# Performance work log

Measured on AMD Instinct MI355X. Metric: run time of the kernel, lower is better.

Reference implementation:

```python
import jax, jax.numpy as jnp
import numpy as np

LATENT = 3
POLY = 3
SINDY_DIM = 22  # 3 ones + 3 linear + 6 quad + 10 cubic


def sindy_library(z, poly_order=POLY, latent_dim=LATENT):
    # z: [N, latent_dim] -> [N, sindy_dim]; mirrors the torch loop ordering.
    N = z.shape[0]
    cols = [jnp.ones((N,), z.dtype) for _ in range(latent_dim)]
    if poly_order > 0:
        cols += [z[:, i] for i in range(latent_dim)]
    if poly_order > 1:
        for i in range(latent_dim):
            for j in range(i, latent_dim):
                cols.append(z[:, i] * z[:, j])
    if poly_order > 2:
        for i in range(latent_dim):
            for j in range(i, latent_dim):
                for k in range(j, latent_dim):
                    cols.append(z[:, i] * z[:, j] * z[:, k])
    return jnp.stack(cols, axis=1)


def _xavier(key, out_f, in_f):
    lim = np.sqrt(6.0 / (in_f + out_f)).astype(np.float32)
    return jax.random.uniform(key, (out_f, in_f), jnp.float32, -lim, lim)


def setup_inputs() -> dict:
    key = jax.random.key(0)
    ks = jax.random.split(key, 16)
    N, D = 262144, 128
    we = [128, 64, 32, 3]
    wd = [3, 32, 64, 128]
    d = {}
    d["x"] = jax.random.normal(ks[0], (N, D), jnp.float32)
    d["dx"] = jax.random.normal(ks[1], (N, D), jnp.float32)
    for li, (i_f, o_f) in enumerate(zip(we[:-1], we[1:])):
        d[f"We{li+1}"] = _xavier(ks[2 + li], o_f, i_f)
        d[f"be{li+1}"] = jnp.zeros((o_f,), jnp.float32)
    for li, (i_f, o_f) in enumerate(zip(wd[:-1], wd[1:])):
        d[f"Wd{li+1}"] = _xavier(ks[6 + li], o_f, i_f)
        d[f"bd{li+1}"] = jnp.zeros((o_f,), jnp.float32)
    d["EW"] = jnp.full((LATENT, SINDY_DIM), 0.5, jnp.float32)  # nn.init.constant_(E.weight, 0.5)
    d["Eb"] = jax.random.normal(ks[10], (LATENT,), jnp.float32) * 0.1
    return d


def reference(x, dx, We1, be1, We2, be2, We3, be3,
              Wd1, bd1, Wd2, bd2, Wd3, bd3, EW, Eb):
    # encoder forward (Linear + Identity chain)
    z = ((x @ We1.T + be1) @ We2.T + be2) @ We3.T + be3            # [N, L]
    # encoder Jacobian is constant (pure linear chain): J_enc = We3 @ We2 @ We1
    J_enc = We3 @ We2 @ We1                                        # [L, D]
    dz = dx @ J_enc.T                                              # [N, L]
    # SINDy prediction of z-dot
    theta = sindy_library(z)                                       # [N, SINDY_DIM]
    dzb = theta @ EW.T + Eb                                        # [N, L]
    # decoder forward
    xb = ((z @ Wd1.T + bd1) @ Wd2.T + bd2) @ Wd3.T + bd3           # [N, D]
    # decoder Jacobian (constant)
    J_dec = Wd3 @ Wd2 @ Wd1                                        # [D, L]
    dxb = dzb @ J_dec.T                                            # [N, D]
    return z, dz, dzb, xb, dxb
```

## Files before the change

kernel.cpp:

```cpp
#include <hip/hip_runtime.h>

#define D 128
#define LAT 3
#define SD 22

__global__ __launch_bounds__(256) void fuse_weights(
    const float* __restrict__ We1, const float* __restrict__ be1,
    const float* __restrict__ We2, const float* __restrict__ be2,
    const float* __restrict__ We3, const float* __restrict__ be3,
    const float* __restrict__ Wd1, const float* __restrict__ bd1,
    const float* __restrict__ Wd2, const float* __restrict__ bd2,
    const float* __restrict__ Wd3, const float* __restrict__ bd3,
    float* __restrict__ ws)
{
    __shared__ float A1[3][64];
    __shared__ float B1[64][3];
    __shared__ float t2d[64];
    const int t = threadIdx.x;

    if (t < 192) {
        {
            int r = t >> 6, c = t & 63;
            float s = 0.f;
            #pragma unroll 8
            for (int i = 0; i < 32; ++i) s += We3[r * 32 + i] * We2[i * 64 + c];
            A1[r][c] = s;
        }
        {
            int o = t / 3, l = t - o * 3;
            float s = 0.f;
            #pragma unroll 8
            for (int i = 0; i < 32; ++i) s += Wd2[o * 32 + i] * Wd1[i * 3 + l];
            B1[o][l] = s;
        }
    } else {
        int i = t - 192;
        float s = bd2[i];
        #pragma unroll 8
        for (int j = 0; j < 32; ++j) s += Wd2[i * 32 + j] * bd1[j];
        t2d[i] = s;
    }
    __syncthreads();

    for (int e = t; e < 3 * D; e += 256) {
        int r = e >> 7, c = e & 127;
        float s = 0.f;
        #pragma unroll 8
        for (int j = 0; j < 64; ++j) s += A1[r][j] * We1[j * D + c];
        ws[e] = s;
    }
    if (t < 3) {
        float s = be3[t];
        #pragma unroll 8
        for (int j = 0; j < 64; ++j) s += A1[t][j] * be1[j];
        #pragma unroll 8
        for (int i = 0; i < 32; ++i) s += We3[t * 32 + i] * be2[i];
        ws[384 + t] = s;
    }
    if (t < 128) {
        float s0 = 0.f, s1 = 0.f, s2 = 0.f, sb = bd3[t];
        #pragma unroll 8
        for (int j = 0; j < 64; ++j) {
            float w = Wd3[t * 64 + j];
            s0 += w * B1[j][0];
            s1 += w * B1[j][1];
            s2 += w * B1[j][2];
            sb += w * t2d[j];
        }
        ((float4*)(ws + 512))[t] = make_float4(s0, s1, s2, sb);
    }
}

__global__ __launch_bounds__(256) void sindy_fused(
    const float* __restrict__ x, const float* __restrict__ dx,
    const float* __restrict__ EW, const float* __restrict__ Eb,
    const float* __restrict__ ws, float* __restrict__ out, int nrows)
{
    const int lane = threadIdx.x & 31;
    const int half = threadIdx.x >> 5;

    const float4 je0 = *(const float4*)(ws + 0 * D + lane * 4);
    const float4 je1 = *(const float4*)(ws + 1 * D + lane * 4);
    const float4 je2 = *(const float4*)(ws + 2 * D + lane * 4);
    const float benc0 = ws[384], benc1 = ws[385], benc2 = ws[386];
    const float4 jd0 = ((const float4*)(ws + 512))[lane * 4 + 0];
    const float4 jd1 = ((const float4*)(ws + 512))[lane * 4 + 1];
    const float4 jd2 = ((const float4*)(ws + 512))[lane * 4 + 2];
    const float4 jd3 = ((const float4*)(ws + 512))[lane * 4 + 3];

    float ew[LAT][SD];
    #pragma unroll
    for (int r = 0; r < LAT; ++r)
        #pragma unroll
        for (int k = 0; k < SD; ++k) ew[r][k] = EW[r * SD + k];
    const float eb0 = Eb[0], eb1 = Eb[1], eb2 = Eb[2];

    const int xbBase  = 9 * nrows;
    const int dxbBase = 137 * nrows;
    const int rowsPerGrid = gridDim.x * 8;

    for (int row = blockIdx.x * 8 + half; row < nrows; row += rowsPerGrid) {
        const float4 xv  = *(const float4*)(x  + row * D + lane * 4);
        const float4 dxv = *(const float4*)(dx + row * D + lane * 4);

        float pz0 = je0.x * xv.x + je0.y * xv.y + je0.z * xv.z + je0.w * xv.w;
        float pz1 = je1.x * xv.x + je1.y * xv.y + je1.z * xv.z + je1.w * xv.w;
        float pz2 = je2.x * xv.x + je2.y * xv.y + je2.z * xv.z + je2.w * xv.w;
        float pd0 = je0.x * dxv.x + je0.y * dxv.y + je0.z * dxv.z + je0.w * dxv.w;
        float pd1 = je1.x * dxv.x + je1.y * dxv.y + je1.z * dxv.z + je1.w * dxv.w;
        float pd2 = je2.x * dxv.x + je2.y * dxv.y + je2.z * dxv.z + je2.w * dxv.w;

        #pragma unroll
        for (int m = 16; m >= 1; m >>= 1) {
            pz0 += __shfl_xor(pz0, m);
            pz1 += __shfl_xor(pz1, m);
            pz2 += __shfl_xor(pz2, m);
            pd0 += __shfl_xor(pd0, m);
            pd1 += __shfl_xor(pd1, m);
            pd2 += __shfl_xor(pd2, m);
        }

        const float z0 = pz0 + benc0, z1 = pz1 + benc1, z2 = pz2 + benc2;

        const float q00 = z0 * z0, q01 = z0 * z1, q02 = z0 * z2;
        const float q11 = z1 * z1, q12 = z1 * z2, q22 = z2 * z2;
        float th[SD];
        th[0] = 1.f;  th[1] = 1.f;  th[2] = 1.f;
        th[3] = z0;   th[4] = z1;   th[5] = z2;
        th[6] = q00;  th[7] = q01;  th[8] = q02;
        th[9] = q11;  th[10] = q12; th[11] = q22;
        th[12] = q00 * z0; th[13] = q00 * z1; th[14] = q00 * z2;
        th[15] = q11 * z0; th[16] = q12 * z0; th[17] = q22 * z0;
        th[18] = q11 * z1; th[19] = q11 * z2; th[20] = q22 * z1;
        th[21] = q22 * z2;

        float dzb0 = eb0, dzb1 = eb1, dzb2 = eb2;
        #pragma unroll
        for (int k = 0; k < SD; ++k) {
            dzb0 += ew[0][k] * th[k];
            dzb1 += ew[1][k] * th[k];
            dzb2 += ew[2][k] * th[k];
        }

        const int n3 = row * 3;
        if (lane < 3) {
            const float zv = (lane == 0) ? z0 : (lane == 1) ? z1 : z2;
            const float dv = (lane == 0) ? pd0 : (lane == 1) ? pd1 : pd2;
            const float bv = (lane == 0) ? dzb0 : (lane == 1) ? dzb1 : dzb2;
            out[n3 + lane] = zv;
            out[3 * nrows + n3 + lane] = dv;
            out[6 * nrows + n3 + lane] = bv;
        }

        float4 xbv, dxbv;
        xbv.x = jd0.x * z0 + jd0.y * z1 + jd0.z * z2 + jd0.w;
        xbv.y = jd1.x * z0 + jd1.y * z1 + jd1.z * z2 + jd1.w;
        xbv.z = jd2.x * z0 + jd2.y * z1 + jd2.z * z2 + jd2.w;
        xbv.w = jd3.x * z0 + jd3.y * z1 + jd3.z * z2 + jd3.w;
        dxbv.x = jd0.x * dzb0 + jd0.y * dzb1 + jd0.z * dzb2;
        dxbv.y = jd1.x * dzb0 + jd1.y * dzb1 + jd1.z * dzb2;
        dxbv.z = jd2.x * dzb0 + jd2.y * dzb1 + jd2.z * dzb2;
        dxbv.w = jd3.x * dzb0 + jd3.y * dzb1 + jd3.z * dzb2;

        *(float4*)(out + xbBase  + row * D + lane * 4) = xbv;
        *(float4*)(out + dxbBase + row * D + lane * 4) = dxbv;
    }
}

extern "C" void kernel_launch(void* const* d_in, const int* in_sizes, int n_in,
                              void* d_out, int out_size, void* d_ws, size_t ws_size,
                              hipStream_t stream) {
    const float* x   = (const float*)d_in[0];
    const float* dx  = (const float*)d_in[1];
    const float* We1 = (const float*)d_in[2];
    const float* be1 = (const float*)d_in[3];
    const float* We2 = (const float*)d_in[4];
    const float* be2 = (const float*)d_in[5];
    const float* We3 = (const float*)d_in[6];
    const float* be3 = (const float*)d_in[7];
    const float* Wd1 = (const float*)d_in[8];
    const float* bd1 = (const float*)d_in[9];
    const float* Wd2 = (const float*)d_in[10];
    const float* bd2 = (const float*)d_in[11];
    const float* Wd3 = (const float*)d_in[12];
    const float* bd3 = (const float*)d_in[13];
    const float* EW  = (const float*)d_in[14];
    const float* Eb  = (const float*)d_in[15];

    float* ws  = (float*)d_ws;
    float* out = (float*)d_out;
    const int nrows = in_sizes[0] / D;

    fuse_weights<<<1, 256, 0, stream>>>(We1, be1, We2, be2, We3, be3,
                                        Wd1, bd1, Wd2, bd2, Wd3, bd3, ws);

    sindy_fused<<<2048, 256, 0, stream>>>(x, dx, EW, Eb, ws, out, nrows);
}
```

Measured before the change: 129.0 us.

## Process two rows per half-wave with register-prefetched next iteration loads

Each 32-lane group now handles two rows per iteration (r and r+8) and the block covers 16 rows per step. The x/dx loads for the next iteration are issued before the current rows are computed, a software-pipelined double buffer held in registers. The goal is to hide global load latency in this bandwidth-bound kernel and to interleave two independent shuffle reductions. In exchange it raises register pressure, which can lower occupancy, and the grid stride doubles while the launch size stays the same.

Result: no change. 130.3 us (+1.0%).

```diff
diff --git a/kernel.cpp b/kernel.cpp
--- a/kernel.cpp
+++ b/kernel.cpp
@@ -71,6 +71,45 @@
     }
 }
 
+
+#define EMIT_ROW(ROW, Z0, Z1, Z2, DV0, DV1, DV2)                              \
+  {                                                                           \
+    const float z0 = (Z0) + benc0, z1 = (Z1) + benc1, z2 = (Z2) + benc2;      \
+    const float q00 = z0*z0, q01 = z0*z1, q02 = z0*z2;                        \
+    const float q11 = z1*z1, q12 = z1*z2, q22 = z2*z2;                        \
+    float th[SD];                                                             \
+    th[0]=1.f; th[1]=1.f; th[2]=1.f;                                          \
+    th[3]=z0;  th[4]=z1;  th[5]=z2;                                           \
+    th[6]=q00; th[7]=q01; th[8]=q02; th[9]=q11; th[10]=q12; th[11]=q22;       \
+    th[12]=q00*z0; th[13]=q00*z1; th[14]=q00*z2;                              \
+    th[15]=q11*z0; th[16]=q12*z0; th[17]=q22*z0;                              \
+    th[18]=q11*z1; th[19]=q11*z2; th[20]=q22*z1; th[21]=q22*z2;               \
+    float b0 = eb0, b1 = eb1, b2 = eb2;                                       \
+    _Pragma("unroll")                                                         \
+    for (int k = 0; k < SD; ++k) {                                            \
+      b0 += ew[0][k]*th[k]; b1 += ew[1][k]*th[k]; b2 += ew[2][k]*th[k];       \
+    }                                                                         \
+    if (lane < 3) {                                                           \
+      const float zv = (lane==0) ? z0   : (lane==1) ? z1   : z2;              \
+      const float dv = (lane==0) ? (DV0): (lane==1) ? (DV1): (DV2);           \
+      const float bv = (lane==0) ? b0   : (lane==1) ? b1   : b2;              \
+      out[(ROW)*3 + lane]             = zv;                                   \
+      out[3*nrows + (ROW)*3 + lane]   = dv;                                   \
+      out[6*nrows + (ROW)*3 + lane]   = bv;                                   \
+    }                                                                         \
+    float4 xbv, dxbv;                                                         \
+    xbv.x  = jd0.x*z0 + jd0.y*z1 + jd0.z*z2 + jd0.w;                          \
+    xbv.y  = jd1.x*z0 + jd1.y*z1 + jd1.z*z2 + jd1.w;                          \
+    xbv.z  = jd2.x*z0 + jd2.y*z1 + jd2.z*z2 + jd2.w;                          \
+    xbv.w  = jd3.x*z0 + jd3.y*z1 + jd3.z*z2 + jd3.w;                          \
+    dxbv.x = jd0.x*b0 + jd0.y*b1 + jd0.z*b2;                                  \
+    dxbv.y = jd1.x*b0 + jd1.y*b1 + jd1.z*b2;                                  \
+    dxbv.z = jd2.x*b0 + jd2.y*b1 + jd2.z*b2;                                  \
+    dxbv.w = jd3.x*b0 + jd3.y*b1 + jd3.z*b2;                                  \
+    *(float4*)(out + xbBase  + (ROW)*D + lane*4) = xbv;                       \
+    *(float4*)(out + dxbBase + (ROW)*D + lane*4) = dxbv;                      \
+  }
+
 __global__ __launch_bounds__(256) void sindy_fused(
     const float* __restrict__ x, const float* __restrict__ dx,
     const float* __restrict__ EW, const float* __restrict__ Eb,
@@ -97,73 +136,62 @@
 
     const int xbBase  = 9 * nrows;
     const int dxbBase = 137 * nrows;
-    const int rowsPerGrid = gridDim.x * 8;
-
-    for (int row = blockIdx.x * 8 + half; row < nrows; row += rowsPerGrid) {
-        const float4 xv  = *(const float4*)(x  + row * D + lane * 4);
-        const float4 dxv = *(const float4*)(dx + row * D + lane * 4);
-
-        float pz0 = je0.x * xv.x + je0.y * xv.y + je0.z * xv.z + je0.w * xv.w;
-        float pz1 = je1.x * xv.x + je1.y * xv.y + je1.z * xv.z + je1.w * xv.w;
-        float pz2 = je2.x * xv.x + je2.y * xv.y + je2.z * xv.z + je2.w * xv.w;
-        float pd0 = je0.x * dxv.x + je0.y * dxv.y + je0.z * dxv.z + je0.w * dxv.w;
-        float pd1 = je1.x * dxv.x + je1.y * dxv.y + je1.z * dxv.z + je1.w * dxv.w;
-        float pd2 = je2.x * dxv.x + je2.y * dxv.y + je2.z * dxv.z + je2.w * dxv.w;
+    const int stride  = gridDim.x * 16;
+
+    int r = blockIdx.x * 16 + half;
+
+    float4 cxa, cda, cxb, cdb;
+    if (r < nrows) {
+        cxa = *(const float4*)(x  + r * D + lane * 4);
+        cda = *(const float4*)(dx + r * D + lane * 4);
+    }
+    if (r + 8 < nrows) {
+        cxb = *(const float4*)(x  + (r + 8) * D + lane * 4);
+        cdb = *(const float4*)(dx + (r + 8) * D + lane * 4);
+    }
+
+    while (r < nrows) {
+        const int nr = r + stride;
+        float4 nxa = cxa, nda = cda, nxb = cxb, ndb = cdb;
+        if (nr < nrows) {
+            nxa = *(const float4*)(x  + nr * D + lane * 4);
+            nda = *(const float4*)(dx + nr * D + lane * 4);
+        }
+        if (nr + 8 < nrows) {
+            nxb = *(const float4*)(x  + (nr + 8) * D + lane * 4);
+            ndb = *(const float4*)(dx + (nr + 8) * D + lane * 4);
+        }
+
+        float za0 = je0.x*cxa.x + je0.y*cxa.y + je0.z*cxa.z + je0.w*cxa.w;
+        float za1 = je1.x*cxa.x + je1.y*cxa.y + je1.z*cxa.z + je1.w*cxa.w;
+        float za2 = je2.x*cxa.x + je2.y*cxa.y + je2.z*cxa.z + je2.w*cxa.w;
+        float da0 = je0.x*cda.x + je0.y*cda.y + je0.z*cda.z + je0.w*cda.w;
+        float da1 = je1.x*cda.x + je1.y*cda.y + je1.z*cda.z + je1.w*cda.w;
+        float da2 = je2.x*cda.x + je2.y*cda.y + je2.z*cda.z + je2.w*cda.w;
+        float zb0 = je0.x*cxb.x + je0.y*cxb.y + je0.z*cxb.z + je0.w*cxb.w;
+        float zb1 = je1.x*cxb.x + je1.y*cxb.y + je1.z*cxb.z + je1.w*cxb.w;
+        float zb2 = je2.x*cxb.x + je2.y*cxb.y + je2.z*cxb.z + je2.w*cxb.w;
+        float db0 = je0.x*cdb.x + je0.y*cdb.y + je0.z*cdb.z + je0.w*cdb.w;
+        float db1 = je1.x*cdb.x + je1.y*cdb.y + je1.z*cdb.z + je1.w*cdb.w;
+        float db2 = je2.x*cdb.x + je2.y*cdb.y + je2.z*cdb.z + je2.w*cdb.w;
 
         #pragma unroll
         for (int m = 16; m >= 1; m >>= 1) {
-            pz0 += __shfl_xor(pz0, m);
-            pz1 += __shfl_xor(pz1, m);
-            pz2 += __shfl_xor(pz2, m);
-            pd0 += __shfl_xor(pd0, m);
-            pd1 += __shfl_xor(pd1, m);
-            pd2 += __shfl_xor(pd2, m);
-        }
-
-        const float z0 = pz0 + benc0, z1 = pz1 + benc1, z2 = pz2 + benc2;
-
-        const float q00 = z0 * z0, q01 = z0 * z1, q02 = z0 * z2;
-        const float q11 = z1 * z1, q12 = z1 * z2, q22 = z2 * z2;
-        float th[SD];
-        th[0] = 1.f;  th[1] = 1.f;  th[2] = 1.f;
-        th[3] = z0;   th[4] = z1;   th[5] = z2;
-        th[6] = q00;  th[7] = q01;  th[8] = q02;
-        th[9] = q11;  th[10] = q12; th[11] = q22;
-        th[12] = q00 * z0; th[13] = q00 * z1; th[14] = q00 * z2;
-        th[15] = q11 * z0; th[16] = q12 * z0; th[17] = q22 * z0;
-        th[18] = q11 * z1; th[19] = q11 * z2; th[20] = q22 * z1;
-        th[21] = q22 * z2;
-
-        float dzb0 = eb0, dzb1 = eb1, dzb2 = eb2;
-        #pragma unroll
-        for (int k = 0; k < SD; ++k) {
-            dzb0 += ew[0][k] * th[k];
-            dzb1 += ew[1][k] * th[k];
-            dzb2 += ew[2][k] * th[k];
-        }
-
-        const int n3 = row * 3;
-        if (lane < 3) {
-            const float zv = (lane == 0) ? z0 : (lane == 1) ? z1 : z2;
-            const float dv = (lane == 0) ? pd0 : (lane == 1) ? pd1 : pd2;
-            const float bv = (lane == 0) ? dzb0 : (lane == 1) ? dzb1 : dzb2;
-            out[n3 + lane] = zv;
-            out[3 * nrows + n3 + lane] = dv;
-            out[6 * nrows + n3 + lane] = bv;
-        }
-
-        float4 xbv, dxbv;
-        xbv.x = jd0.x * z0 + jd0.y * z1 + jd0.z * z2 + jd0.w;
-        xbv.y = jd1.x * z0 + jd1.y * z1 + jd1.z * z2 + jd1.w;
-        xbv.z = jd2.x * z0 + jd2.y * z1 + jd2.z * z2 + jd2.w;
-        xbv.w = jd3.x * z0 + jd3.y * z1 + jd3.z * z2 + jd3.w;
-        dxbv.x = jd0.x * dzb0 + jd0.y * dzb1 + jd0.z * dzb2;
-        dxbv.y = jd1.x * dzb0 + jd1.y * dzb1 + jd1.z * dzb2;
-        dxbv.z = jd2.x * dzb0 + jd2.y * dzb1 + jd2.z * dzb2;
-        dxbv.w = jd3.x * dzb0 + jd3.y * dzb1 + jd3.z * dzb2;
-
-        *(float4*)(out + xbBase  + row * D + lane * 4) = xbv;
-        *(float4*)(out + dxbBase + row * D + lane * 4) = dxbv;
+            za0 += __shfl_xor(za0, m);  za1 += __shfl_xor(za1, m);
+            za2 += __shfl_xor(za2, m);  da0 += __shfl_xor(da0, m);
+            da1 += __shfl_xor(da1, m);  da2 += __shfl_xor(da2, m);
+            zb0 += __shfl_xor(zb0, m);  zb1 += __shfl_xor(zb1, m);
+            zb2 += __shfl_xor(zb2, m);  db0 += __shfl_xor(db0, m);
+            db1 += __shfl_xor(db1, m);  db2 += __shfl_xor(db2, m);
+        }
+
+        EMIT_ROW(r, za0, za1, za2, da0, da1, da2);
+        if (r + 8 < nrows) {
+            EMIT_ROW(r + 8, zb0, zb1, zb2, db0, db1, db2);
+        }
+
+        cxa = nxa; cda = nda; cxb = nxb; cdb = ndb;
+        r = nr;
     }
 }
 
```

## Split fused kernel into encoder/SINDy and decoder kernels with nontemporal I/O

Applied to the files above, without the earlier changes.

Splits the single fused streaming kernel into an encoder+SINDy kernel that reads x/dx and writes z, dz, dzb, and a separate decoder kernel that reads z/dzb back and writes xb/dxb. Loads and stores use nontemporal hints, the grid is sized to one block per 128 rows instead of a fixed 2048-block grid-stride loop, and the constant SINDy library columns are folded into the bias. The split is meant to shorten each kernel's critical path and separate the read-heavy and write-heavy phases. It adds a third kernel launch and an extra small round trip through memory for z and dzb.

Measured after the change: 123.1 us. 1.05x faster.

```diff
diff --git a/kernel.cpp b/kernel.cpp
--- a/kernel.cpp
+++ b/kernel.cpp
@@ -1,8 +1,8 @@
 #include <hip/hip_runtime.h>
 
 #define D 128
-#define LAT 3
-#define SD 22
+
+typedef float f32x4 __attribute__((ext_vector_type(4)));
 
 __global__ __launch_bounds__(256) void fuse_weights(
     const float* __restrict__ We1, const float* __restrict__ be1,
@@ -67,11 +67,14 @@
             s2 += w * B1[j][2];
             sb += w * t2d[j];
         }
-        ((float4*)(ws + 512))[t] = make_float4(s0, s1, s2, sb);
-    }
-}
-
-__global__ __launch_bounds__(256) void sindy_fused(
+        ws[512 + t * 4 + 0] = s0;
+        ws[512 + t * 4 + 1] = s1;
+        ws[512 + t * 4 + 2] = s2;
+        ws[512 + t * 4 + 3] = sb;
+    }
+}
+
+__global__ __launch_bounds__(256) void enc_sindy(
     const float* __restrict__ x, const float* __restrict__ dx,
     const float* __restrict__ EW, const float* __restrict__ Eb,
     const float* __restrict__ ws, float* __restrict__ out, int nrows)
@@ -79,91 +82,111 @@
     const int lane = threadIdx.x & 31;
     const int half = threadIdx.x >> 5;
 
-    const float4 je0 = *(const float4*)(ws + 0 * D + lane * 4);
-    const float4 je1 = *(const float4*)(ws + 1 * D + lane * 4);
-    const float4 je2 = *(const float4*)(ws + 2 * D + lane * 4);
+    const f32x4 je0 = *((const f32x4*)(ws + 0 * D) + lane);
+    const f32x4 je1 = *((const f32x4*)(ws + 1 * D) + lane);
+    const f32x4 je2 = *((const f32x4*)(ws + 2 * D) + lane);
     const float benc0 = ws[384], benc1 = ws[385], benc2 = ws[386];
-    const float4 jd0 = ((const float4*)(ws + 512))[lane * 4 + 0];
-    const float4 jd1 = ((const float4*)(ws + 512))[lane * 4 + 1];
-    const float4 jd2 = ((const float4*)(ws + 512))[lane * 4 + 2];
-    const float4 jd3 = ((const float4*)(ws + 512))[lane * 4 + 3];
-
-    float ew[LAT][SD];
+
+    float ew0[19], ew1[19], ew2[19];
     #pragma unroll
-    for (int r = 0; r < LAT; ++r)
-        #pragma unroll
-        for (int k = 0; k < SD; ++k) ew[r][k] = EW[r * SD + k];
-    const float eb0 = Eb[0], eb1 = Eb[1], eb2 = Eb[2];
-
-    const int xbBase  = 9 * nrows;
-    const int dxbBase = 137 * nrows;
-    const int rowsPerGrid = gridDim.x * 8;
-
-    for (int row = blockIdx.x * 8 + half; row < nrows; row += rowsPerGrid) {
-        const float4 xv  = *(const float4*)(x  + row * D + lane * 4);
-        const float4 dxv = *(const float4*)(dx + row * D + lane * 4);
-
-        float pz0 = je0.x * xv.x + je0.y * xv.y + je0.z * xv.z + je0.w * xv.w;
-        float pz1 = je1.x * xv.x + je1.y * xv.y + je1.z * xv.z + je1.w * xv.w;
-        float pz2 = je2.x * xv.x + je2.y * xv.y + je2.z * xv.z + je2.w * xv.w;
-        float pd0 = je0.x * dxv.x + je0.y * dxv.y + je0.z * dxv.z + je0.w * dxv.w;
-        float pd1 = je1.x * dxv.x + je1.y * dxv.y + je1.z * dxv.z + je1.w * dxv.w;
-        float pd2 = je2.x * dxv.x + je2.y * dxv.y + je2.z * dxv.z + je2.w * dxv.w;
+    for (int k = 0; k < 19; ++k) {
+        ew0[k] = EW[ 3 + k];
+        ew1[k] = EW[25 + k];
+        ew2[k] = EW[47 + k];
+    }
+    const float bs0 = Eb[0] + EW[ 0] + EW[ 1] + EW[ 2];
+    const float bs1 = Eb[1] + EW[22] + EW[23] + EW[24];
+    const float bs2 = Eb[2] + EW[44] + EW[45] + EW[46];
+
+    const int base = blockIdx.x * 128;
+
+    for (int i = 0; i < 16; ++i) {
+        const int row = base + i * 8 + half;
+        if (row >= nrows) continue;
+
+        const f32x4 xv  = __builtin_nontemporal_load((const f32x4*)(x  + row * D) + lane);
+        const f32x4 dxv = __builtin_nontemporal_load((const f32x4*)(dx + row * D) + lane);
+
+        float z0 = je0.x*xv.x + je0.y*xv.y + je0.z*xv.z + je0.w*xv.w;
+        float z1 = je1.x*xv.x + je1.y*xv.y + je1.z*xv.z + je1.w*xv.w;
+        float z2 = je2.x*xv.x + je2.y*xv.y + je2.z*xv.z + je2.w*xv.w;
+        float d0 = je0.x*dxv.x + je0.y*dxv.y + je0.z*dxv.z + je0.w*dxv.w;
+        float d1 = je1.x*dxv.x + je1.y*dxv.y + je1.z*dxv.z + je1.w*dxv.w;
+        float d2 = je2.x*dxv.x + je2.y*dxv.y + je2.z*dxv.z + je2.w*dxv.w;
 
         #pragma unroll
         for (int m = 16; m >= 1; m >>= 1) {
-            pz0 += __shfl_xor(pz0, m);
-            pz1 += __shfl_xor(pz1, m);
-            pz2 += __shfl_xor(pz2, m);
-            pd0 += __shfl_xor(pd0, m);
-            pd1 += __shfl_xor(pd1, m);
-            pd2 += __shfl_xor(pd2, m);
-        }
-
-        const float z0 = pz0 + benc0, z1 = pz1 + benc1, z2 = pz2 + benc2;
-
-        const float q00 = z0 * z0, q01 = z0 * z1, q02 = z0 * z2;
-        const float q11 = z1 * z1, q12 = z1 * z2, q22 = z2 * z2;
-        float th[SD];
-        th[0] = 1.f;  th[1] = 1.f;  th[2] = 1.f;
-        th[3] = z0;   th[4] = z1;   th[5] = z2;
-        th[6] = q00;  th[7] = q01;  th[8] = q02;
-        th[9] = q11;  th[10] = q12; th[11] = q22;
-        th[12] = q00 * z0; th[13] = q00 * z1; th[14] = q00 * z2;
-        th[15] = q11 * z0; th[16] = q12 * z0; th[17] = q22 * z0;
-        th[18] = q11 * z1; th[19] = q11 * z2; th[20] = q22 * z1;
-        th[21] = q22 * z2;
-
-        float dzb0 = eb0, dzb1 = eb1, dzb2 = eb2;
-        #pragma unroll
-        for (int k = 0; k < SD; ++k) {
-            dzb0 += ew[0][k] * th[k];
-            dzb1 += ew[1][k] * th[k];
-            dzb2 += ew[2][k] * th[k];
-        }
-
-        const int n3 = row * 3;
+            z0 += __shfl_xor(z0, m);  z1 += __shfl_xor(z1, m);
+            z2 += __shfl_xor(z2, m);  d0 += __shfl_xor(d0, m);
+            d1 += __shfl_xor(d1, m);  d2 += __shfl_xor(d2, m);
+        }
+
+        z0 += benc0; z1 += benc1; z2 += benc2;
+
+        const float q00 = z0*z0, q01 = z0*z1, q02 = z0*z2;
+        const float q11 = z1*z1, q12 = z1*z2, q22 = z2*z2;
+        const float c0 = q00*z0, c1 = q00*z1, c2 = q00*z2;
+        const float c3 = q11*z0, c4 = q12*z0, c5 = q22*z0;
+        const float c6 = q11*z1, c7 = q11*z2, c8 = q22*z1, c9 = q22*z2;
+
+        float b0 = bs0, b1 = bs1, b2 = bs2;
+        #define ACC(K, V) { b0 += ew0[K]*(V); b1 += ew1[K]*(V); b2 += ew2[K]*(V); }
+        ACC(0, z0)  ACC(1, z1)  ACC(2, z2)
+        ACC(3, q00) ACC(4, q01) ACC(5, q02) ACC(6, q11) ACC(7, q12) ACC(8, q22)
+        ACC(9, c0)  ACC(10, c1) ACC(11, c2) ACC(12, c3) ACC(13, c4)
+        ACC(14, c5) ACC(15, c6) ACC(16, c7) ACC(17, c8) ACC(18, c9)
+        #undef ACC
+
         if (lane < 3) {
             const float zv = (lane == 0) ? z0 : (lane == 1) ? z1 : z2;
-            const float dv = (lane == 0) ? pd0 : (lane == 1) ? pd1 : pd2;
-            const float bv = (lane == 0) ? dzb0 : (lane == 1) ? dzb1 : dzb2;
-            out[n3 + lane] = zv;
-            out[3 * nrows + n3 + lane] = dv;
-            out[6 * nrows + n3 + lane] = bv;
-        }
-
-        float4 xbv, dxbv;
-        xbv.x = jd0.x * z0 + jd0.y * z1 + jd0.z * z2 + jd0.w;
-        xbv.y = jd1.x * z0 + jd1.y * z1 + jd1.z * z2 + jd1.w;
-        xbv.z = jd2.x * z0 + jd2.y * z1 + jd2.z * z2 + jd2.w;
-        xbv.w = jd3.x * z0 + jd3.y * z1 + jd3.z * z2 + jd3.w;
-        dxbv.x = jd0.x * dzb0 + jd0.y * dzb1 + jd0.z * dzb2;
-        dxbv.y = jd1.x * dzb0 + jd1.y * dzb1 + jd1.z * dzb2;
-        dxbv.z = jd2.x * dzb0 + jd2.y * dzb1 + jd2.z * dzb2;
-        dxbv.w = jd3.x * dzb0 + jd3.y * dzb1 + jd3.z * dzb2;
-
-        *(float4*)(out + xbBase  + row * D + lane * 4) = xbv;
-        *(float4*)(out + dxbBase + row * D + lane * 4) = dxbv;
+            const float dv = (lane == 0) ? d0 : (lane == 1) ? d1 : d2;
+            const float bv = (lane == 0) ? b0 : (lane == 1) ? b1 : b2;
+            out[row * 3 + lane]             = zv;
+            out[3 * nrows + row * 3 + lane] = dv;
+            out[6 * nrows + row * 3 + lane] = bv;
+        }
+    }
+}
+
+__global__ __launch_bounds__(256) void dec_kernel(
+    const float* __restrict__ ws, const float* __restrict__ zin,
+    const float* __restrict__ dzbin, float* __restrict__ xbout,
+    float* __restrict__ dxbout, int nrows)
+{
+    const int lane = threadIdx.x & 31;
+    const int half = threadIdx.x >> 5;
+
+    const f32x4 jd0 = *((const f32x4*)(ws + 512) + lane * 4 + 0);
+    const f32x4 jd1 = *((const f32x4*)(ws + 512) + lane * 4 + 1);
+    const f32x4 jd2 = *((const f32x4*)(ws + 512) + lane * 4 + 2);
+    const f32x4 jd3 = *((const f32x4*)(ws + 512) + lane * 4 + 3);
+
+    const int base = blockIdx.x * 128;
+
+    #pragma unroll 4
+    for (int i = 0; i < 16; ++i) {
+        const int row = base + i * 8 + half;
+        if (row >= nrows) continue;
+
+        const float z0 = zin[row * 3 + 0];
+        const float z1 = zin[row * 3 + 1];
+        const float z2 = zin[row * 3 + 2];
+        const float b0 = dzbin[row * 3 + 0];
+        const float b1 = dzbin[row * 3 + 1];
+        const float b2 = dzbin[row * 3 + 2];
+
+        f32x4 xbv, dxbv;
+        xbv.x  = jd0.x*z0 + jd0.y*z1 + jd0.z*z2 + jd0.w;
+        xbv.y  = jd1.x*z0 + jd1.y*z1 + jd1.z*z2 + jd1.w;
+        xbv.z  = jd2.x*z0 + jd2.y*z1 + jd2.z*z2 + jd2.w;
+        xbv.w  = jd3.x*z0 + jd3.y*z1 + jd3.z*z2 + jd3.w;
+        dxbv.x = jd0.x*b0 + jd0.y*b1 + jd0.z*b2;
+        dxbv.y = jd1.x*b0 + jd1.y*b1 + jd1.z*b2;
+        dxbv.z = jd2.x*b0 + jd2.y*b1 + jd2.z*b2;
+        dxbv.w = jd3.x*b0 + jd3.y*b1 + jd3.z*b2;
+
+        __builtin_nontemporal_store(xbv,  (f32x4*)(xbout  + row * D) + lane);
+        __builtin_nontemporal_store(dxbv, (f32x4*)(dxbout + row * D) + lane);
     }
 }
 
@@ -190,9 +213,17 @@
     float* ws  = (float*)d_ws;
     float* out = (float*)d_out;
     const int nrows = in_sizes[0] / D;
+    const int nblk  = (nrows + 127) / 128;
 
     fuse_weights<<<1, 256, 0, stream>>>(We1, be1, We2, be2, We3, be3,
                                         Wd1, bd1, Wd2, bd2, Wd3, bd3, ws);
 
-    sindy_fused<<<2048, 256, 0, stream>>>(x, dx, EW, Eb, ws, out, nrows);
-}
+    enc_sindy<<<nblk, 256, 0, stream>>>(x, dx, EW, Eb, ws, out, nrows);
+
+    dec_kernel<<<nblk, 256, 0, stream>>>(ws,
+                                         out,
+                                         out + 6 * (size_t)nrows,
+                                         out + 9 * (size_t)nrows,
+                                         out + 137 * (size_t)nrows,
+                                         nrows);
+}
```
